# Optimization experiments

Hardware: AMD Instinct MI355X
Metric: run time of the kernel (lower is better)

## Reference

```python
import jax, jax.numpy as jnp
import numpy as np

B, S, D = 4, 2048, 1024
E, TOP_K = 8, 2
CAPACITY_FACTOR = 1.1
H = 4 * D  # expert hidden dim


def setup_inputs() -> dict:
    key = jax.random.key(0)
    ks = jax.random.split(key, 12)
    sc = 0.02
    return {
        "x": jax.random.normal(ks[0], (B, S, D), jnp.float32),
        "noise": jax.random.normal(ks[1], (B, S, E), jnp.float32),
        "W_route": jax.random.normal(ks[2], (D, E), jnp.float32) * sc,
        "b_route": jnp.zeros((E,), jnp.float32),
        "W_noise": jax.random.normal(ks[3], (D, E), jnp.float32) * sc,
        "b_noise": jnp.zeros((E,), jnp.float32),
        "W1": jax.random.normal(ks[4], (E, D, H), jnp.float32) * sc,
        "b1": jnp.zeros((E, H), jnp.float32),
        "W2": jax.random.normal(ks[5], (E, H, D), jnp.float32) * sc,
        "b2": jnp.zeros((E, D), jnp.float32),
    }


def reference(x, noise, W_route, b_route, W_noise, b_noise, W1, b1, W2, b2):
    # ---- NoisyTopkRouter ----
    logits = x @ W_route + b_route                  # [B,S,E]
    noise_logits = x @ W_noise + b_noise            # [B,S,E]
    noisy = logits + noise * jax.nn.softplus(noise_logits)
    top_vals, top_idx = jax.lax.top_k(noisy, TOP_K)  # [B,S,k]
    probs_k = jax.nn.softmax(top_vals, axis=-1)      # softmax over sparse(-inf elsewhere) == softmax over top-k
    onehot = jax.nn.one_hot(top_idx, E, dtype=x.dtype)          # [B,S,k,E]
    router_probs = jnp.einsum('bske,bsk->bse', onehot, probs_k)  # [B,S,E]
    expert_mask = onehot.sum(axis=-2)                            # [B,S,E] (top_k indices are distinct)
    lb_loss = E * jnp.sum(router_probs.mean(axis=(0, 1)) * expert_mask.mean(axis=(0, 1)))

    # ---- capacity-limited dispatch / expert MLP / combine ----
    T = B * S
    cap = int(T * TOP_K / E * CAPACITY_FACTOR)
    flat_x = x.reshape(T, D)
    flat_gate = router_probs.reshape(T, E)
    mask = expert_mask.reshape(T, E) > 0                         # token selects expert
    pos = jnp.cumsum(mask.astype(jnp.int32), axis=0)             # 1-based slot within expert
    keep = mask & (pos <= cap)                                   # first `cap` tokens per expert (flat order)
    priority = jnp.where(keep, jnp.arange(T)[:, None], T)        # [T,E]
    order = jnp.argsort(priority, axis=0)[:cap]                  # [cap,E] token ids (stable: token order)
    valid = (jnp.take_along_axis(priority, order, axis=0) < T).T  # [E,cap]
    gather_idx = order.T                                         # [E,cap]

    x_e = flat_x[gather_idx]                                     # [E,cap,D]
    h = jax.nn.relu(jnp.einsum('ecd,edh->ech', x_e, W1) + b1[:, None, :])
    out_e = jnp.einsum('ech,ehd->ecd', h, W2) + b2[:, None, :]   # dropout is identity in eval mode
    gate = flat_gate[gather_idx, jnp.arange(E)[:, None]]         # [E,cap]
    weighted = out_e * (gate * valid)[..., None]
    updates = jnp.zeros_like(flat_x).at[gather_idx.reshape(-1)].add(weighted.reshape(-1, D))
    return updates.reshape(B, S, D), lb_loss
```

## Files before the change

### kernel.cpp

```cpp
#include <hip/hip_runtime.h>
#include <hip/hip_bf16.h>

#define D_DIM 1024
#define H_DIM 4096
#define E_NUM 8
#define T_TOK 8192
#define CAPN 2252
#define CAP_PAD 2304
#define MT 9

typedef __attribute__((ext_vector_type(8))) short short8;
typedef __attribute__((ext_vector_type(4))) float f32x4;
typedef __attribute__((ext_vector_type(4))) float f4v;
typedef const __attribute__((address_space(1))) void* gas_ptr;
typedef __attribute__((address_space(3))) void* las_ptr;

__device__ __forceinline__ unsigned short f2bf(float f) {
    __hip_bfloat16 h = __float2bfloat16(f);
    return __builtin_bit_cast(unsigned short, h);
}

__global__ void router_kernel(const float* __restrict__ x,
                              const float* __restrict__ noise,
                              const float* __restrict__ Wr,
                              const float* __restrict__ br,
                              const float* __restrict__ Wn,
                              const float* __restrict__ bn,
                              __hip_bfloat16* __restrict__ xb,
                              int* __restrict__ tok_e,
                              float* __restrict__ tok_g)
{
    const int l = threadIdx.x & 63;
    const int w = threadIdx.x >> 6;
    const int t = blockIdx.x * 4 + w;
    const float* xr = x + (size_t)t * D_DIM;

    float ar[8] = {0,0,0,0,0,0,0,0};
    float an[8] = {0,0,0,0,0,0,0,0};
#pragma unroll
    for (int i = 0; i < 4; ++i) {
        int d = i * 256 + l * 4;
        f4v xv = __builtin_nontemporal_load((const f4v*)(xr + d));
        ushort4 xq;
        xq.x = f2bf(xv.x); xq.y = f2bf(xv.y); xq.z = f2bf(xv.z); xq.w = f2bf(xv.w);
        *(ushort4*)(xb + (size_t)t * D_DIM + d) = xq;
        float xs[4] = {xv.x, xv.y, xv.z, xv.w};
#pragma unroll
        for (int j = 0; j < 4; ++j) {
            const float* wrp = Wr + (size_t)(d + j) * 8;
            float4 wa = *(const float4*)wrp;
            float4 wb = *(const float4*)(wrp + 4);
            ar[0] = fmaf(xs[j], wa.x, ar[0]); ar[1] = fmaf(xs[j], wa.y, ar[1]);
            ar[2] = fmaf(xs[j], wa.z, ar[2]); ar[3] = fmaf(xs[j], wa.w, ar[3]);
            ar[4] = fmaf(xs[j], wb.x, ar[4]); ar[5] = fmaf(xs[j], wb.y, ar[5]);
            ar[6] = fmaf(xs[j], wb.z, ar[6]); ar[7] = fmaf(xs[j], wb.w, ar[7]);
            const float* wnp = Wn + (size_t)(d + j) * 8;
            float4 na = *(const float4*)wnp;
            float4 nb = *(const float4*)(wnp + 4);
            an[0] = fmaf(xs[j], na.x, an[0]); an[1] = fmaf(xs[j], na.y, an[1]);
            an[2] = fmaf(xs[j], na.z, an[2]); an[3] = fmaf(xs[j], na.w, an[3]);
            an[4] = fmaf(xs[j], nb.x, an[4]); an[5] = fmaf(xs[j], nb.y, an[5]);
            an[6] = fmaf(xs[j], nb.z, an[6]); an[7] = fmaf(xs[j], nb.w, an[7]);
        }
    }
#pragma unroll
    for (int e = 0; e < 8; ++e) {
#pragma unroll
        for (int s = 32; s > 0; s >>= 1) {
            ar[e] += __shfl_xor(ar[e], s, 64);
            an[e] += __shfl_xor(an[e], s, 64);
        }
    }
    if (l == 0) {
        float nv[8];
#pragma unroll
        for (int e = 0; e < 8; ++e) {
            float z = an[e] + bn[e];
            float sp = fmaxf(z, 0.f) + log1pf(expf(-fabsf(z)));
            nv[e] = ar[e] + br[e] + noise[(size_t)t * 8 + e] * sp;
        }
        int e0 = 0; float v0 = nv[0];
#pragma unroll
        for (int e = 1; e < 8; ++e) if (nv[e] > v0) { v0 = nv[e]; e0 = e; }
        int e1 = -1; float v1 = -3.4e38f;
#pragma unroll
        for (int e = 0; e < 8; ++e) if (e != e0 && nv[e] > v1) { v1 = nv[e]; e1 = e; }
        float ex = expf(v1 - v0);
        float p0 = 1.f / (1.f + ex);
        float p1 = ex * p0;
        tok_e[2 * t]     = e0; tok_e[2 * t + 1] = e1;
        tok_g[2 * t]     = p0; tok_g[2 * t + 1] = p1;
    }
}

__global__ void scan_kernel(const int* __restrict__ tok_e,
                            const float* __restrict__ tok_g,
                            int* __restrict__ routed,
                            int* __restrict__ inv,
                            int* __restrict__ nkept,
                            float* __restrict__ lb_out)
{
    const int e = threadIdx.x >> 6;
    const int l = threadIdx.x & 63;
    __shared__ float s_g[E_NUM];
    __shared__ int   s_c[E_NUM];

    int run = 0;
    float gsum = 0.f;
    for (int b = 0; b < 8; ++b) {
        int2  ev[16];
        float2 gv[16];
#pragma unroll
        for (int c = 0; c < 16; ++c) {
            int t = (b * 16 + c) * 64 + l;
            ev[c] = ((const int2*)tok_e)[t];
            gv[c] = ((const float2*)tok_g)[t];
        }
#pragma unroll
        for (int c = 0; c < 16; ++c) {
            int t = (b * 16 + c) * 64 + l;
            int j = (ev[c].x == e) ? 0 : ((ev[c].y == e) ? 1 : -1);
            bool sel = (j >= 0);
            unsigned long long m = __ballot(sel);
            if (sel) {
                int pos = run + __popcll(m & ((1ull << l) - 1ull));
                if (pos < CAPN) {
                    routed[e * CAP_PAD + pos] = t;
                    inv[2 * t + j] = e * CAP_PAD + pos;
                }
                gsum += (j == 0) ? gv[c].x : gv[c].y;
            }
            run += __popcll(m);
        }
    }
#pragma unroll
    for (int s = 32; s > 0; s >>= 1) gsum += __shfl_xor(gsum, s, 64);
    int nk = min(run, CAPN);
    for (int s = nk + l; s < CAP_PAD; s += 64) routed[e * CAP_PAD + s] = 0;
    if (l == 0) { nkept[e] = nk; s_g[e] = gsum; s_c[e] = run; }
    __syncthreads();
    if (threadIdx.x == 0) {
        float lb = 0.f;
        for (int ee = 0; ee < E_NUM; ++ee)
            lb += (s_g[ee] / (float)T_TOK) * ((float)s_c[ee] / (float)T_TOK);
        lb_out[0] = lb * (float)E_NUM;
    }
}

__global__ void gather_kernel(const ushort* __restrict__ xb,
                              const int* __restrict__ routed,
                              ushort* __restrict__ xg)
{
    const int dc = blockIdx.x & 127;
    const int e  = blockIdx.x >> 7;
    ushort* dst = xg + (size_t)(e * 128 + dc) * CAP_PAD * 8;
    const int* rte = routed + e * CAP_PAD;
#pragma unroll
    for (int p = 0; p < 9; ++p) {
        int m = p * 256 + threadIdx.x;
        int tok = rte[m];
        ulonglong2 v = *(const ulonglong2*)(xb + (size_t)tok * D_DIM + dc * 8);
        *(ulonglong2*)(dst + (size_t)m * 8) = v;
    }
}

__global__ void chunk_weights(const float* __restrict__ in,
                              ushort* __restrict__ out,
                              int K, int N)
{
    __shared__ float tile[64][65];
    const int e = blockIdx.z;
    const int k0 = blockIdx.y * 64, n0 = blockIdx.x * 64;
    const float* src = in + (size_t)e * K * N;
    ushort* dst = out + (size_t)e * (K / 8) * N * 8;
    const int t = threadIdx.x;
    const int rr = t >> 4, c4 = (t & 15) * 4;
#pragma unroll
    for (int p = 0; p < 4; ++p) {
        int r = p * 16 + rr;
        f4v v = __builtin_nontemporal_load(
            (const f4v*)(src + (size_t)(k0 + r) * N + n0 + c4));
        tile[r][c4]     = v.x; tile[r][c4 + 1] = v.y;
        tile[r][c4 + 2] = v.z; tile[r][c4 + 3] = v.w;
    }
    __syncthreads();
    const int n = t & 63, kc = t >> 6;
#pragma unroll
    for (int p = 0; p < 2; ++p) {
        int kcc = p * 4 + kc;
        ushort g[8];
#pragma unroll
        for (int j = 0; j < 8; ++j) g[j] = f2bf(tile[kcc * 8 + j][n]);
        *(short8*)(dst + ((size_t)(k0 / 8 + kcc) * N + n0 + n) * 8) = *(const short8*)g;
    }
}

template <int MODE>
__global__ __launch_bounds__(256, 2) void ffn_gemm(
    const ushort* __restrict__ A,
    const ushort* __restrict__ Bt,
    const float* __restrict__ bias,
    const int* __restrict__ nkept,
    ushort* __restrict__ outH,
    float*  __restrict__ outP,
    int sshift, int nkt)
{
    constexpr int KD = (MODE == 1) ? D_DIM : H_DIM;
    constexpr int ND = (MODE == 1) ? H_DIM : D_DIM;
    constexpr int NC = KD / 8;
    __shared__ ushort lds[36864];

    unsigned total = gridDim.x * gridDim.y * gridDim.z;
    unsigned flat  = blockIdx.x + gridDim.x * (blockIdx.y + gridDim.y * blockIdx.z);
    unsigned sw    = (flat & 7) * (total >> 3) + (flat >> 3);
    unsigned bn    = sw % gridDim.x;
    unsigned t1    = sw / gridDim.x;
    unsigned bm    = t1 % gridDim.y;
    unsigned bz    = t1 / gridDim.y;

    const int e  = (int)(bz >> sshift);
    const int sp = (int)(bz & ((1u << sshift) - 1u));
    const int m0 = (int)bm * 256, n0 = (int)bn * 128;
    if (m0 >= nkept[e]) return;
    const int kc0 = sp * (nkt << 2);

    const int tid  = threadIdx.x;
    const int lane = tid & 63;
    const int w    = tid >> 6;
    const int aw   = w << 10;
    const int bci  = tid >> 7;
    const int bw   = (w & 1) << 10;

    const size_t sAc = (size_t)CAP_PAD * 8;
    const size_t sBc = (size_t)ND * 8;
    const size_t tsA = 4 * sAc;
    const size_t tsB = 4 * sBc;

    const ushort* Ae = A  + ((size_t)e * NC * CAP_PAD + (size_t)(m0 + tid)) * 8
                          + (size_t)kc0 * sAc;
    const ushort* Be = Bt + ((size_t)e * NC * ND + (size_t)(n0 + (tid & 127))) * 8
                          + (size_t)(kc0 + bci) * sBc;

    auto gl = [&](const ushort* g, int ldsbyte) {
        __builtin_amdgcn_global_load_lds((gas_ptr)g, (las_ptr)((char*)lds + ldsbyte), 16, 0, 0);
    };
    auto issueA = [&](size_t off, int stB) {
        gl(Ae + off,            stB + 0 * 4096 + aw);
        gl(Ae + off + sAc,      stB + 1 * 4096 + aw);
        gl(Ae + off + 2 * sAc,  stB + 2 * 4096 + aw);
        gl(Ae + off + 3 * sAc,  stB + 3 * 4096 + aw);
    };
    auto issueB = [&](size_t off, int stB) {
        gl(Be + off,            stB + 16384 + (0 + bci) * 2048 + bw);
        gl(Be + off + 2 * sBc,  stB + 16384 + (2 + bci) * 2048 + bw);
    };

    issueA(0, 0);        issueB(0, 0);
    issueA(tsA, 24576);  issueB(tsB, 24576);
    asm volatile("s_waitcnt vmcnt(6)" ::: "memory");
    __builtin_amdgcn_s_barrier();

    f32x4 acc[8][4] = {};
    const int wm = (w >> 1) * 128;
    const int wn = (w & 1) * 64;
    const int fr = lane & 15;
    const int fq = lane >> 4;

    int rdS = 0;
    int wrB = 49152;
    size_t oA = 2 * tsA;
    size_t oB = 2 * tsB;

    for (int kt = 0; kt < nkt; ++kt) {
        const ushort* Ard = lds + rdS;
        const ushort* Brd = lds + rdS + 8192;

        short8 af[8], bfr[4];
#pragma unroll
        for (int j = 0; j < 4; ++j)
            bfr[j] = *(const short8*)(Brd + fq * 1024 + (wn + j * 16 + fr) * 8);
#pragma unroll
        for (int i = 0; i < 8; ++i)
            af[i] = *(const short8*)(Ard + fq * 2048 + (wm + i * 16 + fr) * 8);

        issueA(oA, wrB);
        issueB(oB, wrB);

        __builtin_amdgcn_s_setprio(1);
#pragma unroll
        for (int i = 0; i < 8; ++i)
#pragma unroll
            for (int j = 0; j < 4; ++j)
                acc[i][j] = __builtin_amdgcn_mfma_f32_16x16x32_bf16(af[i], bfr[j], acc[i][j], 0, 0, 0);
        __builtin_amdgcn_s_setprio(0);

        asm volatile("s_waitcnt vmcnt(6)" ::: "memory");
        __builtin_amdgcn_s_barrier();

        rdS = (rdS == 24576) ? 0 : rdS + 12288;
        wrB = (wrB == 49152) ? 0 : wrB + 24576;
        if (kt < nkt - 3) { oA += tsA; oB += tsB; }
    }

#pragma unroll
    for (int j = 0; j < 4; ++j) {
        int nc = n0 + wn + j * 16 + fr;
        float bv = (MODE == 1) ? bias[e * ND + nc] : 0.f;
#pragma unroll
        for (int i = 0; i < 8; ++i) {
            int mr = m0 + wm + i * 16 + (fq << 2);
#pragma unroll
            for (int r = 0; r < 4; ++r) {
                float v = acc[i][j][r] + bv;
                if (MODE == 1) {
                    v = fmaxf(v, 0.f);
                    outH[(((size_t)e * 512 + (nc >> 3)) * CAP_PAD + mr + r) * 8 + (nc & 7)] = f2bf(v);
                } else {
                    outP[((size_t)(sp * E_NUM + e) * CAP_PAD + mr + r) * D_DIM + nc] = v;
                }
            }
        }
    }
}

__global__ void combine_kernel(const float* __restrict__ part,
                               const int* __restrict__ inv,
                               const float* __restrict__ tok_g,
                               const float* __restrict__ b2,
                               int S,
                               float* __restrict__ out)
{
    const int t = blockIdx.x;
    const int d = threadIdx.x * 4;
    f4v r = {0.f, 0.f, 0.f, 0.f};
#pragma unroll
    for (int j = 0; j < 2; ++j) {
        int i = inv[2 * t + j];
        if (i >= 0) {
            float g = tok_g[2 * t + j];
            int e = i / CAP_PAD;
            f4v a = *(const f4v*)(b2 + (size_t)e * D_DIM + d);
            for (int s = 0; s < S; ++s) {
                f4v p = __builtin_nontemporal_load(
                    (const f4v*)(part + ((size_t)s * E_NUM * CAP_PAD + i) * D_DIM + d));
                a += p;
            }
            r += g * a;
        }
    }
    __builtin_nontemporal_store(r, (f4v*)(out + (size_t)t * D_DIM + d));
}

extern "C" void kernel_launch(void* const* d_in, const int* in_sizes, int n_in,
                              void* d_out, int out_size, void* d_ws, size_t ws_size,
                              hipStream_t stream)
{
    const float* x  = (const float*)d_in[0];
    const float* nz = (const float*)d_in[1];
    const float* Wr = (const float*)d_in[2];
    const float* br = (const float*)d_in[3];
    const float* Wn = (const float*)d_in[4];
    const float* bn = (const float*)d_in[5];
    const float* W1 = (const float*)d_in[6];
    const float* b1 = (const float*)d_in[7];
    const float* W2 = (const float*)d_in[8];
    const float* b2 = (const float*)d_in[9];
    float* out = (float*)d_out;
    char* ws = (char*)d_ws;

    const size_t sz_w2c = (size_t)E_NUM * (H_DIM / 8) * D_DIM * 8 * 2;
    const size_t sz_h   = (size_t)E_NUM * 512 * CAP_PAD * 8 * 2;
    const size_t o_w2c  = 0;
    const size_t o_h    = o_w2c + sz_w2c;
    const size_t o_sm   = o_h + sz_h;
    const size_t o_dyn  = o_sm + (1u << 20);
    const size_t sz_xg  = (size_t)E_NUM * 128 * CAP_PAD * 8 * 2;
    const size_t sz_xb  = (size_t)T_TOK * D_DIM * 2;
    const size_t sz_w1c = (size_t)E_NUM * (D_DIM / 8) * H_DIM * 8 * 2;
    const size_t sz_p1  = sz_xg + sz_xb + sz_w1c;
    const size_t sz_part1 = (size_t)E_NUM * CAP_PAD * D_DIM * 4;

    int sshift = 1;
    while (sshift > 0) {
        size_t need = o_dyn + ((sz_part1 << sshift) > sz_p1 ? (sz_part1 << sshift) : sz_p1);
        if (need <= ws_size) break;
        --sshift;
    }
    const int S = 1 << sshift;

    ushort* w2c  = (ushort*)(ws + o_w2c);
    ushort* hbuf = (ushort*)(ws + o_h);
    int*    rt   = (int*)(ws + o_sm);
    int*    te   = (int*)(ws + o_sm + 131072);
    float*  tg   = (float*)(ws + o_sm + 262144);
    int*    inv  = (int*)(ws + o_sm + 393216);
    int*    nk   = (int*)(ws + o_sm + 524288);
    ushort* xg   = (ushort*)(ws + o_dyn);
    ushort* xb   = (ushort*)(ws + o_dyn + sz_xg);
    ushort* w1c  = (ushort*)(ws + o_dyn + sz_xg + sz_xb);
    float*  part = (float*)(ws + o_dyn);

    (void)hipMemsetAsync(inv, 0xFF, (size_t)T_TOK * 2 * 4, stream);

    router_kernel<<<T_TOK / 4, 256, 0, stream>>>(x, nz, Wr, br, Wn, bn,
                                                 (__hip_bfloat16*)xb, te, tg);
    scan_kernel<<<1, 512, 0, stream>>>(te, tg, rt, inv, nk, out + (size_t)T_TOK * D_DIM);
    chunk_weights<<<dim3(D_DIM / 64, H_DIM / 64, E_NUM), 256, 0, stream>>>(W2, w2c, H_DIM, D_DIM);
    chunk_weights<<<dim3(H_DIM / 64, D_DIM / 64, E_NUM), 256, 0, stream>>>(W1, w1c, D_DIM, H_DIM);
    gather_kernel<<<E_NUM * 128, 256, 0, stream>>>(xb, rt, xg);

    ffn_gemm<1><<<dim3(H_DIM / 128, MT, E_NUM), 256, 0, stream>>>(
        xg, w1c, b1, nk, hbuf, nullptr, 0, D_DIM / 32);

    ffn_gemm<2><<<dim3(D_DIM / 128, MT, E_NUM << sshift), 256, 0, stream>>>(
        hbuf, w2c, nullptr, nk, nullptr, part, sshift, (H_DIM / 32) >> sshift);

    combine_kernel<<<T_TOK, 256, 0, stream>>>(part, inv, tg, b2, S, out);
}
```

Baseline: 564.8 us.

## Fuse W2 weight conversion into GEMM1 launch and store split-K partials as bf16

```diff
diff --git a/kernel.cpp b/kernel.cpp
--- a/kernel.cpp
+++ b/kernel.cpp
@@ -8,16 +8,22 @@
 #define CAPN 2252
 #define CAP_PAD 2304
 #define MT 9
+#define NG1 2304
 
 typedef __attribute__((ext_vector_type(8))) short short8;
 typedef __attribute__((ext_vector_type(4))) float f32x4;
 typedef __attribute__((ext_vector_type(4))) float f4v;
+typedef __attribute__((ext_vector_type(4))) ushort u16x4;
 typedef const __attribute__((address_space(1))) void* gas_ptr;
 typedef __attribute__((address_space(3))) void* las_ptr;
 
 __device__ __forceinline__ unsigned short f2bf(float f) {
     __hip_bfloat16 h = __float2bfloat16(f);
     return __builtin_bit_cast(unsigned short, h);
+}
+__device__ __forceinline__ float bfu2f(ushort u) {
+    unsigned v = (unsigned)u << 16;
+    return __builtin_bit_cast(float, v);
 }
 
 __global__ void router_kernel(const float* __restrict__ x,
@@ -164,15 +170,19 @@
     }
 }
 
-__global__ void chunk_weights(const float* __restrict__ in,
-                              ushort* __restrict__ out,
-                              int K, int N)
-{
-    __shared__ float tile[64][65];
-    const int e = blockIdx.z;
-    const int k0 = blockIdx.y * 64, n0 = blockIdx.x * 64;
-    const float* src = in + (size_t)e * K * N;
-    ushort* dst = out + (size_t)e * (K / 8) * N * 8;
+__device__ __forceinline__ void chunk_body(const float* __restrict__ src0,
+                                           ushort* __restrict__ dstb,
+                                           int K, int N, unsigned i,
+                                           float (*tile)[65])
+{
+    const int nx = N >> 6;
+    const int bx = i % nx;
+    const unsigned rem = i / nx;
+    const int by = rem % (K >> 6);
+    const int e  = rem / (K >> 6);
+    const int k0 = by * 64, n0 = bx * 64;
+    const float* src = src0 + (size_t)e * K * N;
+    ushort* dst = dstb + (size_t)e * (K / 8) * N * 8;
     const int t = threadIdx.x;
     const int rr = t >> 4, c4 = (t & 15) * 4;
 #pragma unroll
@@ -195,18 +205,145 @@
     }
 }
 
-template <int MODE>
-__global__ __launch_bounds__(256, 2) void ffn_gemm(
+__global__ void chunk_weights(const float* __restrict__ in,
+                              ushort* __restrict__ out, int K, int N)
+{
+    __shared__ float tile[64][65];
+    chunk_body(in, out, K, N, blockIdx.x, tile);
+}
+
+__global__ __launch_bounds__(256, 2) void gemm1_chunk2(
     const ushort* __restrict__ A,
     const ushort* __restrict__ Bt,
     const float* __restrict__ bias,
     const int* __restrict__ nkept,
     ushort* __restrict__ outH,
-    float*  __restrict__ outP,
+    const float* __restrict__ W2,
+    ushort* __restrict__ w2c)
+{
+    __shared__ ushort lds[36864];
+    const unsigned blk = blockIdx.x;
+
+    if (blk >= NG1) {
+        chunk_body(W2, w2c, H_DIM, D_DIM, blk - NG1, (float(*)[65])lds);
+        return;
+    }
+
+    constexpr int ND = H_DIM;
+    constexpr int NC = D_DIM / 8;
+    constexpr int nkt = D_DIM / 32;
+
+    unsigned sw = (blk & 7) * (NG1 >> 3) + (blk >> 3);
+    unsigned bn = sw % (H_DIM / 128);
+    unsigned t1 = sw / (H_DIM / 128);
+    unsigned bm = t1 % MT;
+    unsigned e  = t1 / MT;
+
+    const int m0 = (int)bm * 256, n0 = (int)bn * 128;
+    if (m0 >= nkept[e]) return;
+
+    const int tid  = threadIdx.x;
+    const int lane = tid & 63;
+    const int w    = tid >> 6;
+    const int aw   = w << 10;
+    const int bci  = tid >> 7;
+    const int bw   = (w & 1) << 10;
+
+    const size_t sAc = (size_t)CAP_PAD * 8;
+    const size_t sBc = (size_t)ND * 8;
+    const size_t tsA = 4 * sAc;
+    const size_t tsB = 4 * sBc;
+
+    const ushort* Ae = A  + ((size_t)e * NC * CAP_PAD + (size_t)(m0 + tid)) * 8;
+    const ushort* Be = Bt + ((size_t)e * NC * ND + (size_t)(n0 + (tid & 127))) * 8
+                          + (size_t)bci * sBc;
+
+    auto gl = [&](const ushort* g, int ldsbyte) {
+        __builtin_amdgcn_global_load_lds((gas_ptr)g, (las_ptr)((char*)lds + ldsbyte), 16, 0, 0);
+    };
+    auto issueA = [&](size_t off, int stB) {
+        gl(Ae + off,           stB + 0 * 4096 + aw);
+        gl(Ae + off + sAc,     stB + 1 * 4096 + aw);
+        gl(Ae + off + 2 * sAc, stB + 2 * 4096 + aw);
+        gl(Ae + off + 3 * sAc, stB + 3 * 4096 + aw);
+    };
+    auto issueB = [&](size_t off, int stB) {
+        gl(Be + off,           stB + 16384 + (0 + bci) * 2048 + bw);
+        gl(Be + off + 2 * sBc, stB + 16384 + (2 + bci) * 2048 + bw);
+    };
+
+    issueA(0, 0);        issueB(0, 0);
+    issueA(tsA, 24576);  issueB(tsB, 24576);
+    asm volatile("s_waitcnt vmcnt(6)" ::: "memory");
+    __builtin_amdgcn_s_barrier();
+
+    f32x4 acc[8][4] = {};
+    const int wm = (w >> 1) * 128;
+    const int wn = (w & 1) * 64;
+    const int fr = lane & 15;
+    const int fq = lane >> 4;
+
+    int rdS = 0;
+    int wrB = 49152;
+    size_t oA = 2 * tsA;
+    size_t oB = 2 * tsB;
+
+    for (int kt = 0; kt < nkt; ++kt) {
+        const ushort* Ard = lds + rdS;
+        const ushort* Brd = lds + rdS + 8192;
+
+        short8 af[8], bfr[4];
+#pragma unroll
+        for (int j = 0; j < 4; ++j)
+            bfr[j] = *(const short8*)(Brd + fq * 1024 + (wn + j * 16 + fr) * 8);
+#pragma unroll
+        for (int i = 0; i < 8; ++i)
+            af[i] = *(const short8*)(Ard + fq * 2048 + (wm + i * 16 + fr) * 8);
+
+        issueA(oA, wrB);
+        issueB(oB, wrB);
+
+        __builtin_amdgcn_s_setprio(1);
+#pragma unroll
+        for (int i = 0; i < 8; ++i)
+#pragma unroll
+            for (int j = 0; j < 4; ++j)
+                acc[i][j] = __builtin_amdgcn_mfma_f32_16x16x32_bf16(af[i], bfr[j], acc[i][j], 0, 0, 0);
+        __builtin_amdgcn_s_setprio(0);
+
+        asm volatile("s_waitcnt vmcnt(6)" ::: "memory");
+        __builtin_amdgcn_s_barrier();
+
+        rdS = (rdS == 24576) ? 0 : rdS + 12288;
+        wrB = (wrB == 49152) ? 0 : wrB + 24576;
+        if (kt < nkt - 3) { oA += tsA; oB += tsB; }
+    }
+
+#pragma unroll
+    for (int j = 0; j < 4; ++j) {
+        int nc = n0 + wn + j * 16 + fr;
+        float bv = bias[e * ND + nc];
+#pragma unroll
+        for (int i = 0; i < 8; ++i) {
+            int mr = m0 + wm + i * 16 + (fq << 2);
+#pragma unroll
+            for (int r = 0; r < 4; ++r) {
+                float v = fmaxf(acc[i][j][r] + bv, 0.f);
+                outH[(((size_t)e * 512 + (nc >> 3)) * CAP_PAD + mr + r) * 8 + (nc & 7)] = f2bf(v);
+            }
+        }
+    }
+}
+
+__global__ __launch_bounds__(256, 2) void ffn_gemm2(
+    const ushort* __restrict__ A,
+    const ushort* __restrict__ Bt,
+    const int* __restrict__ nkept,
+    ushort* __restrict__ outP,
     int sshift, int nkt)
 {
-    constexpr int KD = (MODE == 1) ? D_DIM : H_DIM;
-    constexpr int ND = (MODE == 1) ? H_DIM : D_DIM;
+    constexpr int KD = H_DIM;
+    constexpr int ND = D_DIM;
     constexpr int NC = KD / 8;
     __shared__ ushort lds[36864];
 
@@ -245,14 +382,14 @@
         __builtin_amdgcn_global_load_lds((gas_ptr)g, (las_ptr)((char*)lds + ldsbyte), 16, 0, 0);
     };
     auto issueA = [&](size_t off, int stB) {
-        gl(Ae + off,            stB + 0 * 4096 + aw);
-        gl(Ae + off + sAc,      stB + 1 * 4096 + aw);
-        gl(Ae + off + 2 * sAc,  stB + 2 * 4096 + aw);
-        gl(Ae + off + 3 * sAc,  stB + 3 * 4096 + aw);
+        gl(Ae + off,           stB + 0 * 4096 + aw);
+        gl(Ae + off + sAc,     stB + 1 * 4096 + aw);
+        gl(Ae + off + 2 * sAc, stB + 2 * 4096 + aw);
+        gl(Ae + off + 3 * sAc, stB + 3 * 4096 + aw);
     };
     auto issueB = [&](size_t off, int stB) {
-        gl(Be + off,            stB + 16384 + (0 + bci) * 2048 + bw);
-        gl(Be + off + 2 * sBc,  stB + 16384 + (2 + bci) * 2048 + bw);
+        gl(Be + off,           stB + 16384 + (0 + bci) * 2048 + bw);
+        gl(Be + off + 2 * sBc, stB + 16384 + (2 + bci) * 2048 + bw);
     };
 
     issueA(0, 0);        issueB(0, 0);
@@ -305,25 +442,18 @@
 #pragma unroll
     for (int j = 0; j < 4; ++j) {
         int nc = n0 + wn + j * 16 + fr;
-        float bv = (MODE == 1) ? bias[e * ND + nc] : 0.f;
 #pragma unroll
         for (int i = 0; i < 8; ++i) {
             int mr = m0 + wm + i * 16 + (fq << 2);
 #pragma unroll
-            for (int r = 0; r < 4; ++r) {
-                float v = acc[i][j][r] + bv;
-                if (MODE == 1) {
-                    v = fmaxf(v, 0.f);
-                    outH[(((size_t)e * 512 + (nc >> 3)) * CAP_PAD + mr + r) * 8 + (nc & 7)] = f2bf(v);
-                } else {
-                    outP[((size_t)(sp * E_NUM + e) * CAP_PAD + mr + r) * D_DIM + nc] = v;
-                }
-            }
-        }
-    }
-}
-
-__global__ void combine_kernel(const float* __restrict__ part,
+            for (int r = 0; r < 4; ++r)
+                outP[((size_t)(sp * E_NUM + e) * CAP_PAD + mr + r) * D_DIM + nc] =
+                    f2bf(acc[i][j][r]);
+        }
+    }
+}
+
+__global__ void combine_kernel(const ushort* __restrict__ part,
                                const int* __restrict__ inv,
                                const float* __restrict__ tok_g,
                                const float* __restrict__ b2,
@@ -341,9 +471,10 @@
             int e = i / CAP_PAD;
             f4v a = *(const f4v*)(b2 + (size_t)e * D_DIM + d);
             for (int s = 0; s < S; ++s) {
-                f4v p = __builtin_nontemporal_load(
-                    (const f4v*)(part + ((size_t)s * E_NUM * CAP_PAD + i) * D_DIM + d));
-                a += p;
+                u16x4 p = __builtin_nontemporal_load(
+                    (const u16x4*)(part + ((size_t)s * E_NUM * CAP_PAD + i) * D_DIM + d));
+                a.x += bfu2f(p.x); a.y += bfu2f(p.y);
+                a.z += bfu2f(p.z); a.w += bfu2f(p.w);
             }
             r += g * a;
         }
@@ -378,7 +509,7 @@
     const size_t sz_xb  = (size_t)T_TOK * D_DIM * 2;
     const size_t sz_w1c = (size_t)E_NUM * (D_DIM / 8) * H_DIM * 8 * 2;
     const size_t sz_p1  = sz_xg + sz_xb + sz_w1c;
-    const size_t sz_part1 = (size_t)E_NUM * CAP_PAD * D_DIM * 4;
+    const size_t sz_part1 = (size_t)E_NUM * CAP_PAD * D_DIM * 2;
 
     int sshift = 1;
     while (sshift > 0) {
@@ -398,22 +529,21 @@
     ushort* xg   = (ushort*)(ws + o_dyn);
     ushort* xb   = (ushort*)(ws + o_dyn + sz_xg);
     ushort* w1c  = (ushort*)(ws + o_dyn + sz_xg + sz_xb);
-    float*  part = (float*)(ws + o_dyn);
+    ushort* part = (ushort*)(ws + o_dyn);
 
     (void)hipMemsetAsync(inv, 0xFF, (size_t)T_TOK * 2 * 4, stream);
 
     router_kernel<<<T_TOK / 4, 256, 0, stream>>>(x, nz, Wr, br, Wn, bn,
                                                  (__hip_bfloat16*)xb, te, tg);
     scan_kernel<<<1, 512, 0, stream>>>(te, tg, rt, inv, nk, out + (size_t)T_TOK * D_DIM);
-    chunk_weights<<<dim3(D_DIM / 64, H_DIM / 64, E_NUM), 256, 0, stream>>>(W2, w2c, H_DIM, D_DIM);
-    chunk_weights<<<dim3(H_DIM / 64, D_DIM / 64, E_NUM), 256, 0, stream>>>(W1, w1c, D_DIM, H_DIM);
+    chunk_weights<<<(H_DIM / 64) * (D_DIM / 64) * E_NUM, 256, 0, stream>>>(W1, w1c, D_DIM, H_DIM);
     gather_kernel<<<E_NUM * 128, 256, 0, stream>>>(xb, rt, xg);
 
-    ffn_gemm<1><<<dim3(H_DIM / 128, MT, E_NUM), 256, 0, stream>>>(
-        xg, w1c, b1, nk, hbuf, nullptr, 0, D_DIM / 32);
-
-    ffn_gemm<2><<<dim3(D_DIM / 128, MT, E_NUM << sshift), 256, 0, stream>>>(
-        hbuf, w2c, nullptr, nk, nullptr, part, sshift, (H_DIM / 32) >> sshift);
+    gemm1_chunk2<<<NG1 + (D_DIM / 64) * (H_DIM / 64) * E_NUM, 256, 0, stream>>>(
+        xg, w1c, b1, nk, hbuf, W2, w2c);
+
+    ffn_gemm2<<<dim3(D_DIM / 128, MT, E_NUM << sshift), 256, 0, stream>>>(
+        hbuf, w2c, nk, part, sshift, (H_DIM / 32) >> sshift);
 
     combine_kernel<<<T_TOK, 256, 0, stream>>>(part, inv, tg, b2, S, out);
 }
```

New measurement: 532.0 us. 1.06x faster.
